# Performance work log

Measured on AMD Instinct MI355X. Metric: run time of the kernel, lower is better.

Reference implementation:

```python
import jax, jax.numpy as jnp
import numpy as np

NUM_HEADS = 8
DIM = 256  # == out_dim; module implicitly requires dim == out_dim


def setup_inputs() -> dict:
    key = jax.random.key(0)
    k0, k1, k2, k3, k4, k5 = jax.random.split(key, 6)
    B, N, T, dim = 4, 128, 128, DIM
    s = dim ** -0.5
    return {
        "v": jax.random.normal(k0, (B, N, T, dim), dtype=jnp.float32),
        "Wq": jax.random.normal(k1, (dim, dim), dtype=jnp.float32) * s,
        "Wk": jax.random.normal(k2, (dim, dim), dtype=jnp.float32) * s,
        "Wv": jax.random.normal(k3, (dim, dim), dtype=jnp.float32) * s,
        "Wp": jax.random.normal(k4, (dim, dim), dtype=jnp.float32) * s,
        "bp": jax.random.normal(k5, (dim,), dtype=jnp.float32) * 0.01,
    }


def reference(v, Wq, Wk, Wv, Wp, bp):
    B, N, T, dim = v.shape
    H = NUM_HEADS
    hd = dim // H
    scale = hd ** -0.5
    # projections (qkv_bias=False)
    q = (v @ Wq).reshape(B * N, T, H, hd)
    k = (v @ Wk).reshape(B * N, T, H, hd)
    vv = (v @ Wv).reshape(B * N, T, H, hd)
    # NOTE: heads axis is NOT moved before the matmul in the original torch
    # code, so attention is over the HEADS axis: per (b*n, t) an HxH matrix.
    attn = jnp.einsum('mthd,mtgd->mthg', q, k) * scale  # [B*N, T, H, H]
    attn = jax.nn.softmax(attn, axis=-1)
    x = jnp.einsum('mthg,mtgd->mthd', attn, vv).reshape(B, N, T, dim)
    # output projection (with bias); dropout probs are 0 / eval mode
    return x @ Wp + bp
```

## Files before the change

kernel.cpp:

```cpp
#include <hip/hip_runtime.h>
#include <hip/hip_bf16.h>
#include <math.h>


#define DIMX      256
#define NH        8
#define HD        32
#define TM        32
#define NTHREADS  512
#define QSTRIDE   776
#define KT        8
#define NT_QKV    48

typedef _Float16 f16x8 __attribute__((ext_vector_type(8)));
typedef _Float16 f16x4 __attribute__((ext_vector_type(4)));
typedef _Float16 f16x2 __attribute__((ext_vector_type(2)));
typedef float    f32x4 __attribute__((ext_vector_type(4)));

static __device__ __forceinline__ f16x2 pkrtz(float a, float b) {
    return (f16x2)__builtin_amdgcn_cvt_pkrtz(a, b);
}

__global__ void pack_weights(const float* __restrict__ Wq,
                             const float* __restrict__ Wk,
                             const float* __restrict__ Wv,
                             const float* __restrict__ Wp,
                             _Float16* __restrict__ pk)
{
    const int QKV_FRAGS = NT_QKV * KT * 64;
    int u = blockIdx.x * blockDim.x + threadIdx.x;
    const float* W;
    int nt, kt, lane;
    if (u < QKV_FRAGS) {
        nt = u / (KT * 64); kt = (u / 64) % KT; lane = u % 64;
        if (nt < 16)      { W = Wq; }
        else if (nt < 32) { W = Wk; nt -= 16; }
        else              { W = Wv; nt -= 32; }
    } else {
        int u2 = u - QKV_FRAGS;
        nt = u2 / (KT * 64); kt = (u2 / 64) % KT; lane = u2 % 64;
        W = Wp;
    }
    const int n  = nt * 16 + (lane & 15);
    const int k0 = kt * 32 + (lane >> 4) * 8;
    f16x8 frag;
#pragma unroll
    for (int j = 0; j < 8; ++j)
        frag[j] = (_Float16)W[(size_t)(k0 + j) * DIMX + n];
    *(f16x8*)(pk + (size_t)u * 8) = frag;
}

__global__ __launch_bounds__(NTHREADS, 6)
void fused_attn_mfma(const float* __restrict__ v,
                     const _Float16* __restrict__ Wqkv_pk,
                     const _Float16* __restrict__ Wp_pk,
                     const float* __restrict__ bp,
                     float* __restrict__ out)
{
    __shared__ __align__(16) _Float16 S[TM * QSTRIDE];

    const int tid   = threadIdx.x;
    const int lane  = tid & 63;
    const int wv_id = tid >> 6;
    const int l15   = lane & 15;
    const int quad  = lane >> 4;
    const long token0 = (long)blockIdx.x * TM;

    {
        const float4* src = (const float4*)(v + token0 * DIMX);
#pragma unroll
        for (int i = 0; i < 4; ++i) {
            int u = tid + NTHREADS * i;
            int m = u >> 6;
            int c = (u & 63) * 4;
            float4 t4 = src[u];
            f16x2 lo = pkrtz(t4.x, t4.y), hi = pkrtz(t4.z, t4.w);
            f16x4 b4 = { lo.x, lo.y, hi.x, hi.y };
            *(f16x4*)&S[m * QSTRIDE + c] = b4;
        }
    }
    __syncthreads();

    f32x4 acc1[2][3];
    int tiles1[3] = { 2 * wv_id, 2 * wv_id + 1, 40 + wv_id };
    {
        int tiles0[3] = { 16 + wv_id * 3, 17 + wv_id * 3, 18 + wv_id * 3 };

        f32x4 acc0[2][3];
#pragma unroll
        for (int tt = 0; tt < 2; ++tt)
#pragma unroll
            for (int j = 0; j < 3; ++j)
                acc0[tt][j] = (f32x4){0.f, 0.f, 0.f, 0.f};
        {
            const f16x8* wb = (const f16x8*)Wqkv_pk + lane;
            f16x8 wcur[3];
#pragma unroll
            for (int j = 0; j < 3; ++j)
                wcur[j] = wb[(size_t)(tiles0[j] * KT) * 64];
            for (int kt = 0; kt < KT; ++kt) {
                const int ktn = (kt + 1 < KT) ? kt + 1 : KT - 1;
                f16x8 wnxt[3];
#pragma unroll
                for (int j = 0; j < 3; ++j)
                    wnxt[j] = wb[(size_t)(tiles0[j] * KT + ktn) * 64];
                f16x8 vf[2];
#pragma unroll
                for (int tt = 0; tt < 2; ++tt)
                    vf[tt] = *(const f16x8*)&S[(tt * 16 + l15) * QSTRIDE + kt * 32 + quad * 8];
#pragma unroll
                for (int j = 0; j < 3; ++j) {
                    acc0[0][j] = __builtin_amdgcn_mfma_f32_16x16x32_f16(wcur[j], vf[0], acc0[0][j], 0, 0, 0);
                    acc0[1][j] = __builtin_amdgcn_mfma_f32_16x16x32_f16(wcur[j], vf[1], acc0[1][j], 0, 0, 0);
                }
#pragma unroll
                for (int j = 0; j < 3; ++j) wcur[j] = wnxt[j];
            }
        }
#pragma unroll
        for (int tt = 0; tt < 2; ++tt)
#pragma unroll
            for (int j = 0; j < 3; ++j) {
                f16x2 a = pkrtz(acc0[tt][j][0], acc0[tt][j][1]);
                f16x2 b = pkrtz(acc0[tt][j][2], acc0[tt][j][3]);
                f16x4 p4 = { a.x, a.y, b.x, b.y };
                *(f16x4*)&S[(tt * 16 + l15) * QSTRIDE + tiles0[j] * 16 + quad * 4] = p4;
            }

#pragma unroll
        for (int tt = 0; tt < 2; ++tt)
#pragma unroll
            for (int j = 0; j < 3; ++j)
                acc1[tt][j] = (f32x4){0.f, 0.f, 0.f, 0.f};
        {
            const f16x8* wb = (const f16x8*)Wqkv_pk + lane;
            f16x8 wcur[3];
#pragma unroll
            for (int j = 0; j < 3; ++j)
                wcur[j] = wb[(size_t)(tiles1[j] * KT) * 64];
            for (int kt = 0; kt < KT; ++kt) {
                const int ktn = (kt + 1 < KT) ? kt + 1 : KT - 1;
                f16x8 wnxt[3];
#pragma unroll
                for (int j = 0; j < 3; ++j)
                    wnxt[j] = wb[(size_t)(tiles1[j] * KT + ktn) * 64];
                f16x8 vf[2];
#pragma unroll
                for (int tt = 0; tt < 2; ++tt)
                    vf[tt] = *(const f16x8*)&S[(tt * 16 + l15) * QSTRIDE + kt * 32 + quad * 8];
#pragma unroll
                for (int j = 0; j < 3; ++j) {
                    acc1[0][j] = __builtin_amdgcn_mfma_f32_16x16x32_f16(wcur[j], vf[0], acc1[0][j], 0, 0, 0);
                    acc1[1][j] = __builtin_amdgcn_mfma_f32_16x16x32_f16(wcur[j], vf[1], acc1[1][j], 0, 0, 0);
                }
#pragma unroll
                for (int j = 0; j < 3; ++j) wcur[j] = wnxt[j];
            }
        }
    }
    __syncthreads();

#pragma unroll
    for (int tt = 0; tt < 2; ++tt)
#pragma unroll
        for (int j = 0; j < 3; ++j) {
            f16x2 a = pkrtz(acc1[tt][j][0], acc1[tt][j][1]);
            f16x2 b = pkrtz(acc1[tt][j][2], acc1[tt][j][3]);
            f16x4 p4 = { a.x, a.y, b.x, b.y };
            *(f16x4*)&S[(tt * 16 + l15) * QSTRIDE + tiles1[j] * 16 + quad * 4] = p4;
        }
    __syncthreads();

    {
        const int ta  = tid >> 4;
        const int sub = tid & 15;
        const int h   = sub >> 1;
        const int d0  = (sub & 1) * 16;
        const float scale = 0.17677669529663687f;

        const _Float16* qrow  = &S[ta * QSTRIDE + h * HD + d0];
        const _Float16* kbase = &S[ta * QSTRIDE + 256 + d0];
        const _Float16* vbase = &S[ta * QSTRIDE + 512 + d0];

        f16x8 q0 = *(const f16x8*)qrow;
        f16x8 q1 = *(const f16x8*)(qrow + 8);

        float logits[NH];
#pragma unroll
        for (int g = 0; g < NH; ++g) {
            f16x8 k0 = *(const f16x8*)(kbase + g * HD);
            f16x8 k1 = *(const f16x8*)(kbase + g * HD + 8);
            f16x8 p  = q0 * k0;
            p += q1 * k1;
            f16x4 r4 = __builtin_shufflevector(p, p, 0, 1, 2, 3)
                     + __builtin_shufflevector(p, p, 4, 5, 6, 7);
            f16x2 r2 = __builtin_shufflevector(r4, r4, 0, 1)
                     + __builtin_shufflevector(r4, r4, 2, 3);
            logits[g] = (float)r2.x + (float)r2.y;
        }
#pragma unroll
        for (int g = 0; g < NH; ++g)
            logits[g] = (logits[g] + __shfl_xor(logits[g], 1, 64)) * scale;

        float mx = logits[0];
#pragma unroll
        for (int g = 1; g < NH; ++g) mx = fmaxf(mx, logits[g]);
        float se = 0.f;
#pragma unroll
        for (int g = 0; g < NH; ++g) { logits[g] = __expf(logits[g] - mx); se += logits[g]; }
        float inv = 1.f / se;

        f16x8 xa0 = (f16x8)(_Float16)0.f;
        f16x8 xa1 = (f16x8)(_Float16)0.f;
#pragma unroll
        for (int g = 0; g < NH; ++g) {
            _Float16 ph = (_Float16)(logits[g] * inv);
            f16x8 pw = { ph, ph, ph, ph, ph, ph, ph, ph };
            f16x8 v0 = *(const f16x8*)(vbase + g * HD);
            f16x8 v1 = *(const f16x8*)(vbase + g * HD + 8);
            xa0 += pw * v0;
            xa1 += pw * v1;
        }
        __syncthreads();
        *(f16x8*)&S[ta * QSTRIDE + h * HD + d0]     = xa0;
        *(f16x8*)&S[ta * QSTRIDE + h * HD + d0 + 8] = xa1;
    }
    __syncthreads();

    {
        const int nt0 = wv_id * 2;
        f32x4 acc[2][2];
#pragma unroll
        for (int tt = 0; tt < 2; ++tt)
#pragma unroll
            for (int j = 0; j < 2; ++j)
                acc[tt][j] = (f32x4){0.f, 0.f, 0.f, 0.f};

        const f16x8* wb = (const f16x8*)Wp_pk + lane;
        f16x8 wcur[2];
#pragma unroll
        for (int j = 0; j < 2; ++j)
            wcur[j] = wb[(size_t)((nt0 + j) * KT) * 64];

        for (int kt = 0; kt < KT; ++kt) {
            const int ktn = (kt + 1 < KT) ? kt + 1 : KT - 1;
            f16x8 wnxt[2];
#pragma unroll
            for (int j = 0; j < 2; ++j)
                wnxt[j] = wb[(size_t)((nt0 + j) * KT + ktn) * 64];
            f16x8 xf[2];
#pragma unroll
            for (int tt = 0; tt < 2; ++tt)
                xf[tt] = *(const f16x8*)&S[(tt * 16 + l15) * QSTRIDE + kt * 32 + quad * 8];
#pragma unroll
            for (int j = 0; j < 2; ++j) {
                acc[0][j] = __builtin_amdgcn_mfma_f32_16x16x32_f16(wcur[j], xf[0], acc[0][j], 0, 0, 0);
                acc[1][j] = __builtin_amdgcn_mfma_f32_16x16x32_f16(wcur[j], xf[1], acc[1][j], 0, 0, 0);
            }
#pragma unroll
            for (int j = 0; j < 2; ++j) wcur[j] = wnxt[j];
        }
#pragma unroll
        for (int j = 0; j < 2; ++j) {
            f32x4 b = *(const f32x4*)&bp[(nt0 + j) * 16 + quad * 4];
#pragma unroll
            for (int tt = 0; tt < 2; ++tt) {
                f32x4 o = acc[tt][j] + b;
                *(f32x4*)&out[(token0 + tt * 16 + l15) * DIMX + (nt0 + j) * 16 + quad * 4] = o;
            }
        }
    }
}

extern "C" void kernel_launch(void* const* d_in, const int* in_sizes, int n_in,
                              void* d_out, int out_size, void* d_ws, size_t ws_size,
                              hipStream_t stream) {
    const float* v  = (const float*)d_in[0];
    const float* Wq = (const float*)d_in[1];
    const float* Wk = (const float*)d_in[2];
    const float* Wv = (const float*)d_in[3];
    const float* Wp = (const float*)d_in[4];
    const float* bp = (const float*)d_in[5];
    float* out = (float*)d_out;

    _Float16* pk = (_Float16*)d_ws;
    const _Float16* Wqkv_pk = pk;
    const _Float16* Wp_pk   = pk + (size_t)24576 * 8;

    pack_weights<<<256, 128, 0, stream>>>(Wq, Wk, Wv, Wp, pk);

    const int ntokens = in_sizes[0] / DIMX;
    fused_attn_mfma<<<ntokens / TM, NTHREADS, 0, stream>>>(v, Wqkv_pk, Wp_pk, bp, out);
}
```

Measured before the change: 158.7 us.

## Keep Q in registers and shrink shared row stride to cut LDS footprint

Reassigns MFMA output tiles so each wave owns one head's Q columns and matching K/V halves. Q stays in registers as fp16 fragments instead of going through shared memory. The shared row stride drops from 776 to 520 halves by reusing the input region for V and staging the last tiles after a barrier. The attention step now uses the MFMA lane layout with cross-lane shuffles and fp32 accumulation. This cuts LDS use per block, which may allow more resident blocks, at the cost of extra shuffles and register pressure.

```diff
diff --git a/kernel.cpp b/kernel.cpp
--- a/kernel.cpp
+++ b/kernel.cpp
@@ -8,7 +8,7 @@
 #define HD        32
 #define TM        32
 #define NTHREADS  512
-#define QSTRIDE   776
+#define QS        520
 #define KT        8
 #define NT_QKV    48
 
@@ -19,6 +19,10 @@
 
 static __device__ __forceinline__ f16x2 pkrtz(float a, float b) {
     return (f16x2)__builtin_amdgcn_cvt_pkrtz(a, b);
+}
+static __device__ __forceinline__ f16x4 pk4(const f32x4& a) {
+    f16x2 lo = pkrtz(a[0], a[1]), hi = pkrtz(a[2], a[3]);
+    return (f16x4){ lo.x, lo.y, hi.x, hi.y };
 }
 
 __global__ void pack_weights(const float* __restrict__ Wq,
@@ -57,7 +61,7 @@
                      const float* __restrict__ bp,
                      float* __restrict__ out)
 {
-    __shared__ __align__(16) _Float16 S[TM * QSTRIDE];
+    __shared__ __align__(16) _Float16 S[TM * QS];
 
     const int tid   = threadIdx.x;
     const int lane  = tid & 63;
@@ -65,6 +69,12 @@
     const int l15   = lane & 15;
     const int quad  = lane >> 4;
     const long token0 = (long)blockIdx.x * TM;
+
+    const int tiles0[3] = { 16 + 2 * wv_id, 17 + 2 * wv_id, 32 + 2 * wv_id };
+    const int tiles1[3] = { 2 * wv_id, 2 * wv_id + 1, 33 + 2 * wv_id };
+
+    const f16x8* wb  = (const f16x8*)Wqkv_pk + lane;
+    const f16x8* wb2 = (const f16x8*)Wp_pk + lane;
 
     {
         const float4* src = (const float4*)(v + token0 * DIMX);
@@ -76,154 +86,154 @@
             float4 t4 = src[u];
             f16x2 lo = pkrtz(t4.x, t4.y), hi = pkrtz(t4.z, t4.w);
             f16x4 b4 = { lo.x, lo.y, hi.x, hi.y };
-            *(f16x4*)&S[m * QSTRIDE + c] = b4;
-        }
-    }
-    __syncthreads();
-
-    f32x4 acc1[2][3];
-    int tiles1[3] = { 2 * wv_id, 2 * wv_id + 1, 40 + wv_id };
-    {
-        int tiles0[3] = { 16 + wv_id * 3, 17 + wv_id * 3, 18 + wv_id * 3 };
-
+            *(f16x4*)&S[m * QS + 256 + c] = b4;
+        }
+    }
+    __syncthreads();
+
+    f16x4 pend0[2];
+    {
         f32x4 acc0[2][3];
 #pragma unroll
         for (int tt = 0; tt < 2; ++tt)
 #pragma unroll
             for (int j = 0; j < 3; ++j)
                 acc0[tt][j] = (f32x4){0.f, 0.f, 0.f, 0.f};
-        {
-            const f16x8* wb = (const f16x8*)Wqkv_pk + lane;
-            f16x8 wcur[3];
+
+        f16x8 wcur[3];
+#pragma unroll
+        for (int j = 0; j < 3; ++j)
+            wcur[j] = wb[(size_t)(tiles0[j] * KT) * 64];
+        for (int kt = 0; kt < KT; ++kt) {
+            const int ktn = (kt + 1 < KT) ? kt + 1 : KT - 1;
+            f16x8 wnxt[3];
 #pragma unroll
             for (int j = 0; j < 3; ++j)
-                wcur[j] = wb[(size_t)(tiles0[j] * KT) * 64];
-            for (int kt = 0; kt < KT; ++kt) {
-                const int ktn = (kt + 1 < KT) ? kt + 1 : KT - 1;
-                f16x8 wnxt[3];
-#pragma unroll
-                for (int j = 0; j < 3; ++j)
-                    wnxt[j] = wb[(size_t)(tiles0[j] * KT + ktn) * 64];
-                f16x8 vf[2];
-#pragma unroll
-                for (int tt = 0; tt < 2; ++tt)
-                    vf[tt] = *(const f16x8*)&S[(tt * 16 + l15) * QSTRIDE + kt * 32 + quad * 8];
-#pragma unroll
-                for (int j = 0; j < 3; ++j) {
-                    acc0[0][j] = __builtin_amdgcn_mfma_f32_16x16x32_f16(wcur[j], vf[0], acc0[0][j], 0, 0, 0);
-                    acc0[1][j] = __builtin_amdgcn_mfma_f32_16x16x32_f16(wcur[j], vf[1], acc0[1][j], 0, 0, 0);
-                }
-#pragma unroll
-                for (int j = 0; j < 3; ++j) wcur[j] = wnxt[j];
-            }
+                wnxt[j] = wb[(size_t)(tiles0[j] * KT + ktn) * 64];
+            f16x8 vf[2];
+#pragma unroll
+            for (int tt = 0; tt < 2; ++tt)
+                vf[tt] = *(const f16x8*)&S[(tt * 16 + l15) * QS + 256 + kt * 32 + quad * 8];
+#pragma unroll
+            for (int j = 0; j < 3; ++j) {
+                acc0[0][j] = __builtin_amdgcn_mfma_f32_16x16x32_f16(wcur[j], vf[0], acc0[0][j], 0, 0, 0);
+                acc0[1][j] = __builtin_amdgcn_mfma_f32_16x16x32_f16(wcur[j], vf[1], acc0[1][j], 0, 0, 0);
+            }
+#pragma unroll
+            for (int j = 0; j < 3; ++j) wcur[j] = wnxt[j];
         }
 #pragma unroll
         for (int tt = 0; tt < 2; ++tt)
 #pragma unroll
-            for (int j = 0; j < 3; ++j) {
-                f16x2 a = pkrtz(acc0[tt][j][0], acc0[tt][j][1]);
-                f16x2 b = pkrtz(acc0[tt][j][2], acc0[tt][j][3]);
-                f16x4 p4 = { a.x, a.y, b.x, b.y };
-                *(f16x4*)&S[(tt * 16 + l15) * QSTRIDE + tiles0[j] * 16 + quad * 4] = p4;
-            }
-
+            for (int j = 0; j < 2; ++j)
+                *(f16x4*)&S[(tt * 16 + l15) * QS + (tiles0[j] - 16) * 16 + quad * 4] = pk4(acc0[tt][j]);
+#pragma unroll
+        for (int tt = 0; tt < 2; ++tt) pend0[tt] = pk4(acc0[tt][2]);
+    }
+
+    f16x4 qf0[2], qf1[2], pend1[2];
+    {
+        f32x4 acc1[2][3];
 #pragma unroll
         for (int tt = 0; tt < 2; ++tt)
 #pragma unroll
             for (int j = 0; j < 3; ++j)
                 acc1[tt][j] = (f32x4){0.f, 0.f, 0.f, 0.f};
-        {
-            const f16x8* wb = (const f16x8*)Wqkv_pk + lane;
-            f16x8 wcur[3];
+
+        f16x8 wcur[3];
+#pragma unroll
+        for (int j = 0; j < 3; ++j)
+            wcur[j] = wb[(size_t)(tiles1[j] * KT) * 64];
+        for (int kt = 0; kt < KT; ++kt) {
+            const int ktn = (kt + 1 < KT) ? kt + 1 : KT - 1;
+            f16x8 wnxt[3];
 #pragma unroll
             for (int j = 0; j < 3; ++j)
-                wcur[j] = wb[(size_t)(tiles1[j] * KT) * 64];
-            for (int kt = 0; kt < KT; ++kt) {
-                const int ktn = (kt + 1 < KT) ? kt + 1 : KT - 1;
-                f16x8 wnxt[3];
-#pragma unroll
-                for (int j = 0; j < 3; ++j)
-                    wnxt[j] = wb[(size_t)(tiles1[j] * KT + ktn) * 64];
-                f16x8 vf[2];
-#pragma unroll
-                for (int tt = 0; tt < 2; ++tt)
-                    vf[tt] = *(const f16x8*)&S[(tt * 16 + l15) * QSTRIDE + kt * 32 + quad * 8];
-#pragma unroll
-                for (int j = 0; j < 3; ++j) {
-                    acc1[0][j] = __builtin_amdgcn_mfma_f32_16x16x32_f16(wcur[j], vf[0], acc1[0][j], 0, 0, 0);
-                    acc1[1][j] = __builtin_amdgcn_mfma_f32_16x16x32_f16(wcur[j], vf[1], acc1[1][j], 0, 0, 0);
+                wnxt[j] = wb[(size_t)(tiles1[j] * KT + ktn) * 64];
+            f16x8 vf[2];
+#pragma unroll
+            for (int tt = 0; tt < 2; ++tt)
+                vf[tt] = *(const f16x8*)&S[(tt * 16 + l15) * QS + 256 + kt * 32 + quad * 8];
+#pragma unroll
+            for (int j = 0; j < 3; ++j) {
+                acc1[0][j] = __builtin_amdgcn_mfma_f32_16x16x32_f16(wcur[j], vf[0], acc1[0][j], 0, 0, 0);
+                acc1[1][j] = __builtin_amdgcn_mfma_f32_16x16x32_f16(wcur[j], vf[1], acc1[1][j], 0, 0, 0);
+            }
+#pragma unroll
+            for (int j = 0; j < 3; ++j) wcur[j] = wnxt[j];
+        }
+#pragma unroll
+        for (int tt = 0; tt < 2; ++tt) {
+            qf0[tt]   = pk4(acc1[tt][0]);
+            qf1[tt]   = pk4(acc1[tt][1]);
+            pend1[tt] = pk4(acc1[tt][2]);
+        }
+    }
+    __syncthreads();
+
+#pragma unroll
+    for (int tt = 0; tt < 2; ++tt) {
+        *(f16x4*)&S[(tt * 16 + l15) * QS + 256 + 32 * wv_id + quad * 4]      = pend0[tt];
+        *(f16x4*)&S[(tt * 16 + l15) * QS + 256 + 32 * wv_id + 16 + quad * 4] = pend1[tt];
+    }
+    __syncthreads();
+
+    f16x4 xq0[2], xq1[2];
+    {
+        const float scale = 0.17677669529663687f;
+#pragma unroll
+        for (int tt = 0; tt < 2; ++tt) {
+            const int t = tt * 16 + l15;
+            const _Float16* krow = &S[t * QS];
+            const _Float16* vrow = &S[t * QS + 256];
+
+            float lg[NH];
+#pragma unroll
+            for (int g = 0; g < NH; ++g) {
+                f16x4 ka = *(const f16x4*)&krow[g * HD + quad * 4];
+                f16x4 kb = *(const f16x4*)&krow[g * HD + 16 + quad * 4];
+                float p = 0.f;
+#pragma unroll
+                for (int r = 0; r < 4; ++r)
+                    p += (float)qf0[tt][r] * (float)ka[r]
+                       + (float)qf1[tt][r] * (float)kb[r];
+                p += __shfl_xor(p, 16, 64);
+                p += __shfl_xor(p, 32, 64);
+                lg[g] = p * scale;
+            }
+            float mx = lg[0];
+#pragma unroll
+            for (int g = 1; g < NH; ++g) mx = fmaxf(mx, lg[g]);
+            float se = 0.f;
+#pragma unroll
+            for (int g = 0; g < NH; ++g) { lg[g] = __expf(lg[g] - mx); se += lg[g]; }
+            float inv = 1.f / se;
+
+            float xr0[4] = {0.f, 0.f, 0.f, 0.f};
+            float xr1[4] = {0.f, 0.f, 0.f, 0.f};
+#pragma unroll
+            for (int g = 0; g < NH; ++g) {
+                f16x4 va = *(const f16x4*)&vrow[g * HD + quad * 4];
+                f16x4 vb = *(const f16x4*)&vrow[g * HD + 16 + quad * 4];
+                float w8 = lg[g] * inv;
+#pragma unroll
+                for (int r = 0; r < 4; ++r) {
+                    xr0[r] += w8 * (float)va[r];
+                    xr1[r] += w8 * (float)vb[r];
                 }
-#pragma unroll
-                for (int j = 0; j < 3; ++j) wcur[j] = wnxt[j];
-            }
-        }
-    }
-    __syncthreads();
-
-#pragma unroll
-    for (int tt = 0; tt < 2; ++tt)
-#pragma unroll
-        for (int j = 0; j < 3; ++j) {
-            f16x2 a = pkrtz(acc1[tt][j][0], acc1[tt][j][1]);
-            f16x2 b = pkrtz(acc1[tt][j][2], acc1[tt][j][3]);
-            f16x4 p4 = { a.x, a.y, b.x, b.y };
-            *(f16x4*)&S[(tt * 16 + l15) * QSTRIDE + tiles1[j] * 16 + quad * 4] = p4;
-        }
-    __syncthreads();
-
-    {
-        const int ta  = tid >> 4;
-        const int sub = tid & 15;
-        const int h   = sub >> 1;
-        const int d0  = (sub & 1) * 16;
-        const float scale = 0.17677669529663687f;
-
-        const _Float16* qrow  = &S[ta * QSTRIDE + h * HD + d0];
-        const _Float16* kbase = &S[ta * QSTRIDE + 256 + d0];
-        const _Float16* vbase = &S[ta * QSTRIDE + 512 + d0];
-
-        f16x8 q0 = *(const f16x8*)qrow;
-        f16x8 q1 = *(const f16x8*)(qrow + 8);
-
-        float logits[NH];
-#pragma unroll
-        for (int g = 0; g < NH; ++g) {
-            f16x8 k0 = *(const f16x8*)(kbase + g * HD);
-            f16x8 k1 = *(const f16x8*)(kbase + g * HD + 8);
-            f16x8 p  = q0 * k0;
-            p += q1 * k1;
-            f16x4 r4 = __builtin_shufflevector(p, p, 0, 1, 2, 3)
-                     + __builtin_shufflevector(p, p, 4, 5, 6, 7);
-            f16x2 r2 = __builtin_shufflevector(r4, r4, 0, 1)
-                     + __builtin_shufflevector(r4, r4, 2, 3);
-            logits[g] = (float)r2.x + (float)r2.y;
-        }
-#pragma unroll
-        for (int g = 0; g < NH; ++g)
-            logits[g] = (logits[g] + __shfl_xor(logits[g], 1, 64)) * scale;
-
-        float mx = logits[0];
-#pragma unroll
-        for (int g = 1; g < NH; ++g) mx = fmaxf(mx, logits[g]);
-        float se = 0.f;
-#pragma unroll
-        for (int g = 0; g < NH; ++g) { logits[g] = __expf(logits[g] - mx); se += logits[g]; }
-        float inv = 1.f / se;
-
-        f16x8 xa0 = (f16x8)(_Float16)0.f;
-        f16x8 xa1 = (f16x8)(_Float16)0.f;
-#pragma unroll
-        for (int g = 0; g < NH; ++g) {
-            _Float16 ph = (_Float16)(logits[g] * inv);
-            f16x8 pw = { ph, ph, ph, ph, ph, ph, ph, ph };
-            f16x8 v0 = *(const f16x8*)(vbase + g * HD);
-            f16x8 v1 = *(const f16x8*)(vbase + g * HD + 8);
-            xa0 += pw * v0;
-            xa1 += pw * v1;
-        }
-        __syncthreads();
-        *(f16x8*)&S[ta * QSTRIDE + h * HD + d0]     = xa0;
-        *(f16x8*)&S[ta * QSTRIDE + h * HD + d0 + 8] = xa1;
+            }
+            f16x2 a0 = pkrtz(xr0[0], xr0[1]), b0 = pkrtz(xr0[2], xr0[3]);
+            f16x2 a1 = pkrtz(xr1[0], xr1[1]), b1 = pkrtz(xr1[2], xr1[3]);
+            xq0[tt] = (f16x4){ a0.x, a0.y, b0.x, b0.y };
+            xq1[tt] = (f16x4){ a1.x, a1.y, b1.x, b1.y };
+        }
+    }
+    __syncthreads();
+#pragma unroll
+    for (int tt = 0; tt < 2; ++tt) {
+        const int t = tt * 16 + l15;
+        *(f16x4*)&S[t * QS + 32 * wv_id + quad * 4]      = xq0[tt];
+        *(f16x4*)&S[t * QS + 32 * wv_id + 16 + quad * 4] = xq1[tt];
     }
     __syncthreads();
 
@@ -236,22 +246,20 @@
             for (int j = 0; j < 2; ++j)
                 acc[tt][j] = (f32x4){0.f, 0.f, 0.f, 0.f};
 
-        const f16x8* wb = (const f16x8*)Wp_pk + lane;
         f16x8 wcur[2];
 #pragma unroll
         for (int j = 0; j < 2; ++j)
-            wcur[j] = wb[(size_t)((nt0 + j) * KT) * 64];
-
+            wcur[j] = wb2[(size_t)((nt0 + j) * KT) * 64];
         for (int kt = 0; kt < KT; ++kt) {
             const int ktn = (kt + 1 < KT) ? kt + 1 : KT - 1;
             f16x8 wnxt[2];
 #pragma unroll
             for (int j = 0; j < 2; ++j)
-                wnxt[j] = wb[(size_t)((nt0 + j) * KT + ktn) * 64];
+                wnxt[j] = wb2[(size_t)((nt0 + j) * KT + ktn) * 64];
             f16x8 xf[2];
 #pragma unroll
             for (int tt = 0; tt < 2; ++tt)
-                xf[tt] = *(const f16x8*)&S[(tt * 16 + l15) * QSTRIDE + kt * 32 + quad * 8];
+                xf[tt] = *(const f16x8*)&S[(tt * 16 + l15) * QS + kt * 32 + quad * 8];
 #pragma unroll
             for (int j = 0; j < 2; ++j) {
                 acc[0][j] = __builtin_amdgcn_mfma_f32_16x16x32_f16(wcur[j], xf[0], acc[0][j], 0, 0, 0);
```

Result: slower. 194.3 us (+22.5%).
